# Kernel optimization log

Hardware: AMD Instinct MI355X
Metric: run time of the kernel (lower is better)

The kernel has to match this reference:

```python
import jax, jax.numpy as jnp
import numpy as np

N_NODES = 25000
N_HEDGES = 12500
NNZ = 400000
C_IN = 128
HID = 256
HEADS = 4
DH = HID // HEADS  # 64
NQ = 1             # number_queries
LN_EPS = 1e-5


def _layer_norm(x, g, b):
    m = jnp.mean(x, axis=-1, keepdims=True)
    v = jnp.mean((x - m) ** 2, axis=-1, keepdims=True)
    return (x - m) * jax.lax.rsqrt(v + LN_EPS) * g + b


def _block(x_src, src, tgt, n_tgt, K, Qw, V, ln0_g, ln0_b, ln1_g, ln1_b, W1, W2):
    """AllSetTransformerBlock: segment-softmax multi-head attention + LN/MLP.

    x_src: [N_src, C]; K,V: [H, C, DH]; Qw: [H, NQ, DH]; src,tgt: [E] int.
    torch.sparse.softmax over dim=1 == softmax over each target's incident
    sources (unspecified entries are -inf), so a segment softmax is exact.
    """
    xK = jnp.einsum('nc,hcd->hnd', x_src, K)        # [H, N, DH]
    alpha = jnp.einsum('hqd,hnd->nhq', Qw, xK)      # [N, H, NQ]
    a = alpha[src]                                   # [E, H, NQ] gather per incidence
    m = jax.ops.segment_max(a, tgt, num_segments=n_tgt)
    e = jnp.exp(a - m[tgt])
    den = jax.ops.segment_sum(e, tgt, num_segments=n_tgt)
    attn = e / den[tgt]                              # [E, H, NQ]
    v = jnp.einsum('nc,hcd->nhd', x_src, V)[src]     # [E, H, DH]
    w = attn[:, :, :, None] * v[:, :, None, :]       # [E, H, NQ, DH]
    out = jax.ops.segment_sum(w, tgt, num_segments=n_tgt)  # [T, H, NQ, DH]
    out = out + Qw[None]                             # residual with queries
    out = out.transpose(0, 2, 1, 3).reshape(n_tgt, NQ, HID)
    x = _layer_norm(out, ln0_g, ln0_b)
    h = jnp.maximum(x @ W1, 0.0) @ W2                # MLP: Linear-ReLU-Linear, no bias
    x = _layer_norm(x + jnp.maximum(h, 0.0), ln1_g, ln1_b)
    return x.sum(axis=1)                             # [T, HID]


def setup_inputs() -> dict:
    key = jax.random.key(0)
    ks = jax.random.split(key, 12)
    # injective linear-congruential index generation -> unique (node, hedge) pairs,
    # matching a coalesced sparse incidence matrix
    P = 15485863
    lin = (np.arange(NNZ, dtype=np.int64) * P) % (N_NODES * N_HEDGES)
    node_idx = jnp.asarray(lin // N_HEDGES, dtype=jnp.int64)
    hedge_idx = jnp.asarray(lin % N_HEDGES, dtype=jnp.int64)
    s = 0.05
    w = lambda k, shape: jax.random.normal(k, shape, jnp.float32) * s
    d = {
        'x0': jax.random.normal(ks[0], (N_NODES, C_IN), jnp.float32),
        'node_idx': node_idx,
        'hedge_idx': hedge_idx,
        'n_hedges': N_HEDGES,
        'v2e_K': w(ks[1], (HEADS, C_IN, DH)),
        'v2e_Q': w(ks[2], (HEADS, NQ, DH)),
        'v2e_V': w(ks[3], (HEADS, C_IN, DH)),
        'v2e_W1': w(ks[4], (HID, HID)),
        'v2e_W2': w(ks[5], (HID, HID)),
        'v2e_ln0_g': jnp.ones(HID, jnp.float32), 'v2e_ln0_b': jnp.zeros(HID, jnp.float32),
        'v2e_ln1_g': jnp.ones(HID, jnp.float32), 'v2e_ln1_b': jnp.zeros(HID, jnp.float32),
        'e2v_K': w(ks[6], (HEADS, HID, DH)),
        'e2v_Q': w(ks[7], (HEADS, NQ, DH)),
        'e2v_V': w(ks[8], (HEADS, HID, DH)),
        'e2v_W1': w(ks[9], (HID, HID)),
        'e2v_W2': w(ks[10], (HID, HID)),
        'e2v_ln0_g': jnp.ones(HID, jnp.float32), 'e2v_ln0_b': jnp.zeros(HID, jnp.float32),
        'e2v_ln1_g': jnp.ones(HID, jnp.float32), 'e2v_ln1_b': jnp.zeros(HID, jnp.float32),
    }
    return d


def reference(x0, node_idx, hedge_idx, n_hedges,
              v2e_K, v2e_Q, v2e_V, v2e_W1, v2e_W2,
              v2e_ln0_g, v2e_ln0_b, v2e_ln1_g, v2e_ln1_b,
              e2v_K, e2v_Q, e2v_V, e2v_W1, e2v_W2,
              e2v_ln0_g, e2v_ln0_b, e2v_ln1_g, e2v_ln1_b):
    n_nodes = x0.shape[0]
    # vertex -> hyperedge (neighborhood = B^T: targets are hyperedges)
    x1 = jax.nn.relu(_block(x0, node_idx, hedge_idx, n_hedges,
                            v2e_K, v2e_Q, v2e_V,
                            v2e_ln0_g, v2e_ln0_b, v2e_ln1_g, v2e_ln1_b,
                            v2e_W1, v2e_W2))
    # hyperedge -> vertex (neighborhood = B: targets are nodes)
    x0_out = jax.nn.relu(_block(x1, hedge_idx, node_idx, n_nodes,
                                e2v_K, e2v_Q, e2v_V,
                                e2v_ln0_g, e2v_ln0_b, e2v_ln1_g, e2v_ln1_b,
                                e2v_W1, e2v_W2))
    return x0_out, x1
```

## Files before the change

kernel.cpp:

```cpp
#include <hip/hip_runtime.h>
#include <hip/hip_bf16.h>

#define N_NODES_C 25000
#define N_HEDGES_C 12500
#define NNZ_C 400000
#define C_IN_C 128
#define HID_C 256
#define LN_EPS_C 1e-5f
#define CSR_STRIDE 64

typedef unsigned short ushort_t;
typedef __attribute__((ext_vector_type(8))) short short8;
typedef __attribute__((ext_vector_type(4))) float f32x4;

union U4S8 { uint4 u; short8 s; };

__device__ __forceinline__ float ldsel(const void* p, size_t i, bool f32) {
    return f32 ? ((const float*)p)[i] : __bfloat162float(((const __hip_bfloat16*)p)[i]);
}
__device__ __forceinline__ int ldidx(const void* p, size_t i, bool i64) {
    return i64 ? (int)((const long long*)p)[i] : ((const int*)p)[i];
}
__device__ __forceinline__ ushort_t bfbits(float f) {
    union { float f; unsigned u; } v; v.f = f;
    unsigned r = v.u + 0x7FFF + ((v.u >> 16) & 1);
    return (ushort_t)(r >> 16);
}
__device__ __forceinline__ float blo(unsigned u) {
    union { unsigned u; float f; } v; v.u = u << 16; return v.f;
}
__device__ __forceinline__ float bhi(unsigned u) {
    union { unsigned u; float f; } v; v.u = u & 0xFFFF0000u; return v.f;
}

#define INIT_GRID 148
__global__ void __launch_bounds__(256)
init_kernel(const unsigned* __restrict__ x0w, const unsigned* __restrict__ idxw,
            int* __restrict__ flags, unsigned* __restrict__ cnts,
            unsigned* __restrict__ vb32, unsigned* __restrict__ ea32) {
    int bid = blockIdx.x;
    if (bid == 0) {
        __shared__ int cnt[2];
        int t = threadIdx.x;
        if (t < 2) cnt[t] = 0;
        __syncthreads();
        int c0 = 0, c1 = 0;
        for (int k = 0; k < 4; k++) {
            unsigned w = x0w[t * 4 + k];
            unsigned elo = (w >> 7) & 0xFF;
            if (elo >= 100 && elo <= 134) c0++;
            if (idxw[2 * (t * 4 + k) + 1] == 0) c1++;
        }
        atomicAdd(&cnt[0], c0);
        atomicAdd(&cnt[1], c1);
        __syncthreads();
        if (t == 0) {
            flags[0] = (cnt[0] < 512) ? 1 : 0;
            flags[1] = (cnt[1] >= 512) ? 1 : 0;
        }
        return;
    }
    int i = (bid - 1) * 256 + threadIdx.x;
    if (i < 37500) { cnts[i] = 0u; return; }
    i -= 37500;
    if (i < 128) { vb32[25000 * 128 + i] = 0u; return; }
    i -= 128;
    if (i < 4) ea32[100000 + i] = 0u;
}

#define FILL_CHUNK 1024
#define FILL_NCHUNK ((NNZ_C + FILL_CHUNK - 1) / FILL_CHUNK)
#define FILL_BLOCKS (8 * FILL_NCHUNK)
#define HSLICE_SZ 1563
#define NSLICE_SZ 3125
#define PREP_TOTAL 364544
#define PREP_BLOCKS ((PREP_TOTAL + 255) / 256)
#define PF_GRID (FILL_BLOCKS + PREP_BLOCKS)

__global__ void __launch_bounds__(256)
prep_fill_kernel(const void* __restrict__ node_idx, const void* __restrict__ hedge_idx,
                 int* __restrict__ fill_h, int* __restrict__ fill_n,
                 ushort_t* __restrict__ scsr_h, ushort_t* __restrict__ scsr_n,
                 const void* __restrict__ K1, const void* __restrict__ Q1,
                 const void* __restrict__ V1,
                 const void* __restrict__ K2, const void* __restrict__ Q2,
                 const void* __restrict__ V2,
                 const void* __restrict__ W1a, const void* __restrict__ W2a,
                 const void* __restrict__ W1b, const void* __restrict__ W2b,
                 const void* __restrict__ G0a, const void* __restrict__ B0a,
                 const void* __restrict__ G1a, const void* __restrict__ B1a,
                 const void* __restrict__ G0b, const void* __restrict__ B0b,
                 const void* __restrict__ G1b, const void* __restrict__ B1b,
                 const int* __restrict__ flags,
                 float* __restrict__ kq1, float* __restrict__ kq2,
                 ushort_t* __restrict__ Vt1b, ushort_t* __restrict__ Vt2b,
                 ushort_t* __restrict__ W1tA, ushort_t* __restrict__ W2tA,
                 ushort_t* __restrict__ W1tB, ushort_t* __restrict__ W2tB,
                 float* __restrict__ qgb1, float* __restrict__ ep1,
                 float* __restrict__ qgb2, float* __restrict__ ep2) {
    if (blockIdx.x < FILL_BLOCKS) {
        bool i64 = flags[1] != 0;
        int s = blockIdx.x & 7;
        int chunk = blockIdx.x >> 3;
        int e0 = chunk * FILL_CHUNK;
        int e1 = e0 + FILL_CHUNK; if (e1 > NNZ_C) e1 = NNZ_C;
        int hlo = s * HSLICE_SZ, hhi = hlo + HSLICE_SZ;
        int nlo = s * NSLICE_SZ, nhi = nlo + NSLICE_SZ;
        for (int e = e0 + threadIdx.x; e < e1; e += 256) {
            int nd = ldidx(node_idx, e, i64);
            int he = ldidx(hedge_idx, e, i64);
            if (he >= hlo && he < hhi) {
                int p = atomicAdd(&fill_h[he], 1);
                if (p < CSR_STRIDE) scsr_h[(he << 6) + p] = (ushort_t)nd;
            }
            if (nd >= nlo && nd < nhi) {
                int p = atomicAdd(&fill_n[nd], 1);
                if (p < CSR_STRIDE) scsr_n[(nd << 6) + p] = (ushort_t)he;
            }
        }
        return;
    }
    bool f32 = flags[0] != 0;
    size_t i = (size_t)(blockIdx.x - FILL_BLOCKS) * 256 + threadIdx.x;
    if (i >= PREP_TOTAL) return;
    if (i < 512) {
        int h = (int)(i >> 7), c = (int)(i & 127);
        float s = 0.f;
        for (int d = 0; d < 64; d++)
            s += ldsel(K1, (size_t)(h * 128 + c) * 64 + d, f32) * ldsel(Q1, h * 64 + d, f32);
        kq1[h * 128 + c] = s;
        return;
    }
    i -= 512;
    if (i < 1024) {
        int h = (int)(i >> 8), c = (int)(i & 255);
        float s = 0.f;
        for (int d = 0; d < 64; d++)
            s += ldsel(K2, (size_t)(h * 256 + c) * 64 + d, f32) * ldsel(Q2, h * 64 + d, f32);
        kq2[h * 256 + c] = s;
        return;
    }
    i -= 1024;
    if (i < 32768) {
        int j = (int)(i >> 7), c = (int)(i & 127);
        int h = j >> 6, d = j & 63;
        Vt1b[i] = bfbits(ldsel(V1, (size_t)(h * 128 + c) * 64 + d, f32));
        return;
    }
    i -= 32768;
    if (i < 65536) {
        int j = (int)(i >> 8), c = (int)(i & 255);
        int h = j >> 6, d = j & 63;
        Vt2b[i] = bfbits(ldsel(V2, (size_t)(h * 256 + c) * 64 + d, f32));
        return;
    }
    i -= 65536;
    if (i < 65536) { int n = (int)(i >> 8), k = (int)(i & 255);
        W1tA[i] = bfbits(ldsel(W1a, (size_t)k * 256 + n, f32)); return; }
    i -= 65536;
    if (i < 65536) { int n = (int)(i >> 8), k = (int)(i & 255);
        W2tA[i] = bfbits(ldsel(W2a, (size_t)k * 256 + n, f32)); return; }
    i -= 65536;
    if (i < 65536) { int n = (int)(i >> 8), k = (int)(i & 255);
        W1tB[i] = bfbits(ldsel(W1b, (size_t)k * 256 + n, f32)); return; }
    i -= 65536;
    if (i < 65536) { int n = (int)(i >> 8), k = (int)(i & 255);
        W2tB[i] = bfbits(ldsel(W2b, (size_t)k * 256 + n, f32)); return; }
    i -= 65536;
    {
        int which = (int)(i >> 8);
        int j = (int)(i & 255);
        const void* src; float* dst;
        switch (which) {
            case 0: src = Q1;  dst = qgb1;       break;
            case 1: src = G0a; dst = qgb1 + 256; break;
            case 2: src = B0a; dst = qgb1 + 512; break;
            case 3: src = G1a; dst = ep1;        break;
            case 4: src = B1a; dst = ep1 + 256;  break;
            case 5: src = Q2;  dst = qgb2;       break;
            case 6: src = G0b; dst = qgb2 + 256; break;
            case 7: src = B0b; dst = qgb2 + 512; break;
            case 8: src = G1b; dst = ep2;        break;
            default: src = B1b; dst = ep2 + 256;  break;
        }
        dst[j] = ldsel(src, j, f32);
    }
}

__global__ void __launch_bounds__(256)
gemm_x0_kernel(const void* __restrict__ x0, const int* __restrict__ flags,
               const ushort_t* __restrict__ Bt, ushort_t* __restrict__ C,
               int M, int K, const float* __restrict__ kq, float* __restrict__ ea) {
    __shared__ ushort_t As[64 * 72];
    __shared__ ushort_t Bs[128 * 72];
    __shared__ float kqs[512];
    bool f32 = flags[0] != 0;
    int tid = threadIdx.x;
    int w = tid >> 6, lane = tid & 63;
    int l15 = lane & 15, kg = lane >> 4;
    int wr = w >> 1, wc = w & 1;
    int row0 = blockIdx.x * 64, col0 = blockIdx.y * 128;
    bool doEa = (blockIdx.y == 0);
    kqs[tid] = kq[tid];
    kqs[256 + tid] = kq[256 + tid];
    __syncthreads();
    f32x4 acc[2][4] = {{{0.f,0.f,0.f,0.f},{0.f,0.f,0.f,0.f},{0.f,0.f,0.f,0.f},{0.f,0.f,0.f,0.f}},
                       {{0.f,0.f,0.f,0.f},{0.f,0.f,0.f,0.f},{0.f,0.f,0.f,0.f},{0.f,0.f,0.f,0.f}}};
    float hd[2][4] = {{0.f,0.f,0.f,0.f},{0.f,0.f,0.f,0.f}};
    int r_ = tid >> 3, ch = tid & 7;
    for (int k0 = 0; k0 < K; k0 += 64) {
#pragma unroll
        for (int p = 0; p < 2; p++) {
            int r = p * 32 + r_;
            uint4 av = {0u,0u,0u,0u};
            int gr = row0 + r;
            if (gr < M) {
                float fv[8];
                if (!f32) {
                    av = *(const uint4*)((const ushort_t*)x0 + (size_t)gr * K + k0 + ch * 8);
                    if (doEa) {
                        unsigned* uw = (unsigned*)&av;
#pragma unroll
                        for (int jj = 0; jj < 4; jj++) { fv[2 * jj] = blo(uw[jj]); fv[2 * jj + 1] = bhi(uw[jj]); }
                    }
                } else {
                    const float* ap = (const float*)x0 + (size_t)gr * K + k0 + ch * 8;
                    float4 f0 = *(const float4*)ap;
                    float4 f1 = *(const float4*)(ap + 4);
                    av.x = (unsigned)bfbits(f0.x) | ((unsigned)bfbits(f0.y) << 16);
                    av.y = (unsigned)bfbits(f0.z) | ((unsigned)bfbits(f0.w) << 16);
                    av.z = (unsigned)bfbits(f1.x) | ((unsigned)bfbits(f1.y) << 16);
                    av.w = (unsigned)bfbits(f1.z) | ((unsigned)bfbits(f1.w) << 16);
                    if (doEa) {
                        fv[0] = f0.x; fv[1] = f0.y; fv[2] = f0.z; fv[3] = f0.w;
                        fv[4] = f1.x; fv[5] = f1.y; fv[6] = f1.z; fv[7] = f1.w;
                    }
                }
                if (doEa) {
                    int c = k0 + ch * 8;
#pragma unroll
                    for (int h = 0; h < 4; h++) {
                        float s = 0.f;
#pragma unroll
                        for (int j = 0; j < 8; j++) s += fv[j] * kqs[h * 128 + c + j];
                        hd[p][h] += s;
                    }
                }
            }
            *(uint4*)&As[r * 72 + ch * 8] = av;
        }
#pragma unroll
        for (int p = 0; p < 4; p++) {
            int i = p * 256 + tid;
            int r2 = i >> 3, c2 = i & 7;
            uint4 bv = *(const uint4*)(Bt + (size_t)(col0 + r2) * K + k0 + c2 * 8);
            *(uint4*)&Bs[r2 * 72 + c2 * 8] = bv;
        }
        __syncthreads();
#pragma unroll
        for (int kk = 0; kk < 2; kk++) {
            U4S8 a0_, a1_;
            a0_.u = *(const uint4*)&As[(32 * wr + l15) * 72 + kk * 32 + kg * 8];
            a1_.u = *(const uint4*)&As[(32 * wr + 16 + l15) * 72 + kk * 32 + kg * 8];
#pragma unroll
            for (int n = 0; n < 4; n++) {
                U4S8 b; b.u = *(const uint4*)&Bs[(64 * wc + 16 * n + l15) * 72 + kk * 32 + kg * 8];
                acc[0][n] = __builtin_amdgcn_mfma_f32_16x16x32_bf16(a0_.s, b.s, acc[0][n], 0, 0, 0);
                acc[1][n] = __builtin_amdgcn_mfma_f32_16x16x32_bf16(a1_.s, b.s, acc[1][n], 0, 0, 0);
            }
        }
        __syncthreads();
    }
#pragma unroll
    for (int m = 0; m < 2; m++) {
#pragma unroll
        for (int n = 0; n < 4; n++) {
#pragma unroll
            for (int rr = 0; rr < 4; rr++) {
                int row = row0 + 32 * wr + 16 * m + kg * 4 + rr;
                if (row < M)
                    C[(size_t)row * 256 + col0 + 64 * wc + 16 * n + l15] = bfbits(acc[m][n][rr]);
            }
        }
    }
    if (doEa) {
#pragma unroll
        for (int p = 0; p < 2; p++) {
#pragma unroll
            for (int msk = 1; msk < 8; msk <<= 1) {
                hd[p][0] += __shfl_xor(hd[p][0], msk);
                hd[p][1] += __shfl_xor(hd[p][1], msk);
                hd[p][2] += __shfl_xor(hd[p][2], msk);
                hd[p][3] += __shfl_xor(hd[p][3], msk);
            }
            if (ch == 0) {
                int row = row0 + p * 32 + r_;
                if (row < M) {
                    float4 o;
                    o.x = __expf(hd[p][0]); o.y = __expf(hd[p][1]);
                    o.z = __expf(hd[p][2]); o.w = __expf(hd[p][3]);
                    *(float4*)(ea + (size_t)row * 4) = o;
                }
            }
        }
    }
}

#define LOADB4(SRC, KO) { \
    bv0 = *(const uint4*)((SRC) + (size_t)rb * 256 + (KO) + cb * 8); \
    bv1 = *(const uint4*)((SRC) + (size_t)(rb + 64) * 256 + (KO) + cb * 8); \
    bv2 = *(const uint4*)((SRC) + (size_t)(rb + 128) * 256 + (KO) + cb * 8); \
    bv3 = *(const uint4*)((SRC) + (size_t)(rb + 192) * 256 + (KO) + cb * 8); }
#define WRITEB4() { \
    *(uint4*)&Bs[rb * 72 + cb * 8] = bv0; \
    *(uint4*)&Bs[(rb + 64) * 72 + cb * 8] = bv1; \
    *(uint4*)&Bs[(rb + 128) * 72 + cb * 8] = bv2; \
    *(uint4*)&Bs[(rb + 192) * 72 + cb * 8] = bv3; }

__global__ void __launch_bounds__(512)
fused_mlp_ln_kernel(const ushort_t* __restrict__ A, const ushort_t* __restrict__ W1t,
                    const ushort_t* __restrict__ W2t, const float* __restrict__ ep,
                    float* __restrict__ outF, int M,
                    const ushort_t* __restrict__ Vt2b, const float* __restrict__ kq,
                    ushort_t* __restrict__ vbOut, float* __restrict__ eaOut,
                    unsigned* __restrict__ zrow, float* __restrict__ zea) {
    __shared__ ushort_t Bs[256 * 72];
    __shared__ ushort_t hs[32 * 264];
    __shared__ float s1s[32][4];
    __shared__ float s2s[32][4];
    __shared__ float kqs[1024];
    ushort_t* As = hs;
    int tid = threadIdx.x;
    int w = tid >> 6, lane = tid & 63;
    int l15 = lane & 15, kg = lane >> 4;
    int wr = w >> 2, wc = w & 3;
    int row0 = blockIdx.x * 32;
    bool dir1 = (Vt2b != nullptr);
    if (dir1) { kqs[tid] = kq[tid]; kqs[512 + tid] = kq[512 + tid]; }
    f32x4 acc[4] = {{0.f,0.f,0.f,0.f},{0.f,0.f,0.f,0.f},{0.f,0.f,0.f,0.f},{0.f,0.f,0.f,0.f}};
    int rb = tid >> 3, cb = tid & 7;
    bool doA = tid < 256;
    int gr = row0 + rb;
    uint4 av = {0u,0u,0u,0u};
    uint4 bv0, bv1, bv2, bv3;
    LOADB4(W1t, 0);
    if (doA && gr < M) av = *(const uint4*)(A + (size_t)gr * 256 + cb * 8);
    for (int k0 = 0; k0 < 256; k0 += 64) {
        WRITEB4();
        if (doA) *(uint4*)&As[rb * 72 + cb * 8] = av;
        __syncthreads();
        if (k0 < 192) {
            LOADB4(W1t, k0 + 64);
            if (doA && gr < M) av = *(const uint4*)(A + (size_t)gr * 256 + (k0 + 64) + cb * 8);
        }
#pragma unroll
        for (int kk = 0; kk < 2; kk++) {
            U4S8 a0_;
            a0_.u = *(const uint4*)&As[(16 * wr + l15) * 72 + kk * 32 + kg * 8];
#pragma unroll
            for (int n = 0; n < 4; n++) {
                U4S8 b; b.u = *(const uint4*)&Bs[(64 * wc + 16 * n + l15) * 72 + kk * 32 + kg * 8];
                acc[n] = __builtin_amdgcn_mfma_f32_16x16x32_bf16(a0_.s, b.s, acc[n], 0, 0, 0);
            }
        }
        __syncthreads();
    }
    LOADB4(W2t, 0);
#pragma unroll
    for (int n = 0; n < 4; n++) {
#pragma unroll
        for (int rr = 0; rr < 4; rr++) {
            int br = 16 * wr + kg * 4 + rr;
            hs[br * 264 + 64 * wc + 16 * n + l15] = bfbits(fmaxf(acc[n][rr], 0.f));
            acc[n][rr] = 0.f;
        }
    }
    __syncthreads();
    for (int k0 = 0; k0 < 256; k0 += 64) {
        WRITEB4();
        __syncthreads();
        if (k0 < 192) LOADB4(W2t, k0 + 64);
#pragma unroll
        for (int kk = 0; kk < 2; kk++) {
            U4S8 a0_;
            a0_.u = *(const uint4*)&hs[(16 * wr + l15) * 264 + k0 + kk * 32 + kg * 8];
#pragma unroll
            for (int n = 0; n < 4; n++) {
                U4S8 b; b.u = *(const uint4*)&Bs[(64 * wc + 16 * n + l15) * 72 + kk * 32 + kg * 8];
                acc[n] = __builtin_amdgcn_mfma_f32_16x16x32_bf16(a0_.s, b.s, acc[n], 0, 0, 0);
            }
        }
        __syncthreads();
    }
    float ym[4][4];
#pragma unroll
    for (int rr = 0; rr < 4; rr++) {
        int br = 16 * wr + kg * 4 + rr;
        int grow = row0 + br;
        float ls1 = 0.f;
#pragma unroll
        for (int n = 0; n < 4; n++) {
            int col = 64 * wc + 16 * n + l15;
            float xv = 0.f;
            if (grow < M) xv = blo((unsigned)A[(size_t)grow * 256 + col]);
            float yv = xv + fmaxf(acc[n][rr], 0.f);
            ym[n][rr] = yv;
            ls1 += yv;
        }
#pragma unroll
        for (int msk = 1; msk < 16; msk <<= 1) ls1 += __shfl_xor(ls1, msk);
        if (l15 == 0) s1s[br][wc] = ls1;
    }
    __syncthreads();
    float mean_[4];
#pragma unroll
    for (int rr = 0; rr < 4; rr++) {
        int br = 16 * wr + kg * 4 + rr;
        float mn = (s1s[br][0] + s1s[br][1] + s1s[br][2] + s1s[br][3]) * (1.f / 256.f);
        mean_[rr] = mn;
        float ls2 = 0.f;
#pragma unroll
        for (int n = 0; n < 4; n++) {
            float d = ym[n][rr] - mn;
            ls2 += d * d;
        }
#pragma unroll
        for (int msk = 1; msk < 16; msk <<= 1) ls2 += __shfl_xor(ls2, msk);
        if (l15 == 0) s2s[br][wc] = ls2;
    }
    __syncthreads();
#pragma unroll
    for (int rr = 0; rr < 4; rr++) {
        int br = 16 * wr + kg * 4 + rr;
        int grow = row0 + br;
        float var = (s2s[br][0] + s2s[br][1] + s2s[br][2] + s2s[br][3]) * (1.f / 256.f);
        float rs = rsqrtf(var + LN_EPS_C);
#pragma unroll
        for (int n = 0; n < 4; n++) {
            int col = 64 * wc + 16 * n + l15;
            float rv = (ym[n][rr] - mean_[rr]) * rs * ep[col] + ep[256 + col];
            rv = fmaxf(rv, 0.f);
            if (grow < M) outF[(size_t)grow * 256 + col] = rv;
            if (dir1) hs[br * 264 + col] = bfbits(rv);
        }
    }
    if (!dir1) return;
#pragma unroll
    for (int n = 0; n < 4; n++)
#pragma unroll
        for (int rr = 0; rr < 4; rr++) acc[n][rr] = 0.f;
    LOADB4(Vt2b, 0);
    __syncthreads();
    if (blockIdx.x == 0) {
        if (tid < 128) zrow[tid] = 0u;
        else if (tid < 132) zea[tid - 128] = 0.f;
    }
    {
        int rrow = tid >> 4, rch = tid & 15;
        float h0 = 0.f, h1 = 0.f, h2 = 0.f, h3 = 0.f;
#pragma unroll
        for (int q = 0; q < 2; q++) {
            uint4 xv = *(const uint4*)&hs[rrow * 264 + rch * 16 + q * 8];
            const unsigned* uw = (const unsigned*)&xv;
#pragma unroll
            for (int jj = 0; jj < 4; jj++) {
                float xl = blo(uw[jj]), xh = bhi(uw[jj]);
                int c = rch * 16 + q * 8 + jj * 2;
                h0 += xl * kqs[c]       + xh * kqs[c + 1];
                h1 += xl * kqs[256 + c] + xh * kqs[256 + c + 1];
                h2 += xl * kqs[512 + c] + xh * kqs[512 + c + 1];
                h3 += xl * kqs[768 + c] + xh * kqs[768 + c + 1];
            }
        }
#pragma unroll
        for (int msk = 1; msk < 16; msk <<= 1) {
            h0 += __shfl_xor(h0, msk); h1 += __shfl_xor(h1, msk);
            h2 += __shfl_xor(h2, msk); h3 += __shfl_xor(h3, msk);
        }
        int grow = row0 + rrow;
        if (rch == 0 && grow < M) {
            float4 o;
            o.x = __expf(h0); o.y = __expf(h1); o.z = __expf(h2); o.w = __expf(h3);
            *(float4*)(eaOut + (size_t)grow * 4) = o;
        }
    }
    for (int k0 = 0; k0 < 256; k0 += 64) {
        WRITEB4();
        __syncthreads();
        if (k0 < 192) LOADB4(Vt2b, k0 + 64);
#pragma unroll
        for (int kk = 0; kk < 2; kk++) {
            U4S8 a0_;
            a0_.u = *(const uint4*)&hs[(16 * wr + l15) * 264 + k0 + kk * 32 + kg * 8];
#pragma unroll
            for (int n = 0; n < 4; n++) {
                U4S8 b; b.u = *(const uint4*)&Bs[(64 * wc + 16 * n + l15) * 72 + kk * 32 + kg * 8];
                acc[n] = __builtin_amdgcn_mfma_f32_16x16x32_bf16(a0_.s, b.s, acc[n], 0, 0, 0);
            }
        }
        __syncthreads();
    }
#pragma unroll
    for (int n = 0; n < 4; n++) {
#pragma unroll
        for (int rr = 0; rr < 4; rr++) {
            int row = row0 + 16 * wr + kg * 4 + rr;
            if (row < M)
                vbOut[(size_t)row * 256 + 64 * wc + 16 * n + l15] = bfbits(acc[n][rr]);
        }
    }
}

#define DECL_BANKD(B) float e##B##0, e##B##1, e##B##2, e##B##3; \
                      uint2 u##B##0, u##B##1, u##B##2, u##B##3;
#define ISSUED1(B, n, sl) { \
    int _i = ((sl) < cnt) ? __shfl(myidx, (sl)) : dummyIdx; \
    int _o = _i << 9; \
    u##B##n = *(const uint2*)(vbL + _o); \
    e##B##n = *(const float*)(eaL + (_o >> 5)); }
#define ISSUED4(B, base) ISSUED1(B,0,(base)) ISSUED1(B,1,(base)+1) ISSUED1(B,2,(base)+2) ISSUED1(B,3,(base)+3)
#define EATD1(B, n) { \
    float wgt = e##B##n; \
    den += wgt; \
    a0 += wgt * blo(u##B##n.x); a1 += wgt * bhi(u##B##n.x); \
    a2 += wgt * blo(u##B##n.y); a3 += wgt * bhi(u##B##n.y); }
#define EATD4(B) EATD1(B,0) EATD1(B,1) EATD1(B,2) EATD1(B,3)

__global__ void __launch_bounds__(256)
attn_ln_kernel(const int* __restrict__ cnts, const ushort_t* __restrict__ scsr,
               const char* __restrict__ eaB, const char* __restrict__ vbB,
               const float* __restrict__ qgb, uint2* __restrict__ xlnbf2,
               int dummyIdx) {
    int wid = (blockIdx.x << 2) + (threadIdx.x >> 6);
    int lane = threadIdx.x & 63;
    const char* vbL = vbB + (lane << 3);
    const char* eaL = eaB + ((lane >> 4) << 2);
    int cnt = cnts[wid];
    if (cnt > CSR_STRIDE) cnt = CSR_STRIDE;
    int myidx = (int)scsr[(wid << 6) + lane];
    float a0 = 0.f, a1 = 0.f, a2 = 0.f, a3 = 0.f, den = 0.f;
    int kr = (cnt + 3) & ~3;
    DECL_BANKD(A)
    DECL_BANKD(B)
    if (kr > 0) { ISSUED4(A, 0) }
    for (int k = 0; k < kr; k += 8) {
        int kb = k + 4;
        bool hasB = kb < kr;
        if (hasB) { ISSUED4(B, kb) }
        EATD4(A)
        int ka = k + 8;
        if (ka < kr) { ISSUED4(A, ka) }
        if (hasB) { EATD4(B) }
    }
    float inv = (den > 0.f) ? (1.f / den) : 0.f;
    int c0i = lane << 2;
    float o0 = a0 * inv + qgb[c0i];
    float o1 = a1 * inv + qgb[c0i + 1];
    float o2 = a2 * inv + qgb[c0i + 2];
    float o3 = a3 * inv + qgb[c0i + 3];
    float part = o0 + o1 + o2 + o3;
#pragma unroll
    for (int m = 32; m; m >>= 1) part += __shfl_xor(part, m);
    float mean = part * (1.f / 256.f);
    float d0 = o0 - mean, d1 = o1 - mean, d2 = o2 - mean, d3 = o3 - mean;
    float p2 = d0 * d0 + d1 * d1 + d2 * d2 + d3 * d3;
#pragma unroll
    for (int m = 32; m; m >>= 1) p2 += __shfl_xor(p2, m);
    float rs = rsqrtf(p2 * (1.f / 256.f) + LN_EPS_C);
    float r0 = d0 * rs * qgb[256 + c0i] + qgb[512 + c0i];
    float r1 = d1 * rs * qgb[256 + c0i + 1] + qgb[512 + c0i + 1];
    float r2 = d2 * rs * qgb[256 + c0i + 2] + qgb[512 + c0i + 2];
    float r3 = d3 * rs * qgb[256 + c0i + 3] + qgb[512 + c0i + 3];
    uint2 outw;
    outw.x = ((unsigned)bfbits(r1) << 16) | bfbits(r0);
    outw.y = ((unsigned)bfbits(r3) << 16) | bfbits(r2);
    xlnbf2[(size_t)wid * 64 + lane] = outw;
}

#define OFF_KQ1   0
#define OFF_KQ2   2048
#define OFF_QGB1  6144
#define OFF_EP1   9216
#define OFF_QGB2  11264
#define OFF_EP2   14336
#define OFF_EA    16384
#define OFF_VT1B  416512
#define OFF_VT2B  482048
#define OFF_W1TA  613120
#define OFF_W2TA  744192
#define OFF_W1TB  875264
#define OFF_W2TB  1006336
#define OFF_VB    1137408
#define OFF_XLNBF 13937920
#define OFF_FLAGS 45937920
#define OFF_FILLH 45937952
#define OFF_FILLN 45987952
#define OFF_SCSRH 46087952
#define OFF_SCSRN 47687952

extern "C" void kernel_launch(void* const* d_in, const int* in_sizes, int n_in,
                              void* d_out, int out_size, void* d_ws, size_t ws_size,
                              hipStream_t stream) {
    const void* x0        = d_in[0];
    const void* node_idx  = d_in[1];
    const void* hedge_idx = d_in[2];
    const void* v2e_K  = d_in[4];
    const void* v2e_Q  = d_in[5];
    const void* v2e_V  = d_in[6];
    const void* v2e_W1 = d_in[7];
    const void* v2e_W2 = d_in[8];
    const void* v2e_ln0_g = d_in[9];
    const void* v2e_ln0_b = d_in[10];
    const void* v2e_ln1_g = d_in[11];
    const void* v2e_ln1_b = d_in[12];
    const void* e2v_K  = d_in[13];
    const void* e2v_Q  = d_in[14];
    const void* e2v_V  = d_in[15];
    const void* e2v_W1 = d_in[16];
    const void* e2v_W2 = d_in[17];
    const void* e2v_ln0_g = d_in[18];
    const void* e2v_ln0_b = d_in[19];
    const void* e2v_ln1_g = d_in[20];
    const void* e2v_ln1_b = d_in[21];

    float* out = (float*)d_out;
    float* out_x0 = out;
    float* out_x1 = out + (size_t)N_NODES_C * HID_C;

    char* base = (char*)d_ws;
    float*    kq1   = (float*)(base + OFF_KQ1);
    float*    kq2   = (float*)(base + OFF_KQ2);
    float*    qgb1  = (float*)(base + OFF_QGB1);
    float*    ep1   = (float*)(base + OFF_EP1);
    float*    qgb2  = (float*)(base + OFF_QGB2);
    float*    ep2   = (float*)(base + OFF_EP2);
    float*    ea    = (float*)(base + OFF_EA);
    ushort_t* Vt1b  = (ushort_t*)(base + OFF_VT1B);
    ushort_t* Vt2b  = (ushort_t*)(base + OFF_VT2B);
    ushort_t* W1tA  = (ushort_t*)(base + OFF_W1TA);
    ushort_t* W2tA  = (ushort_t*)(base + OFF_W2TA);
    ushort_t* W1tB  = (ushort_t*)(base + OFF_W1TB);
    ushort_t* W2tB  = (ushort_t*)(base + OFF_W2TB);
    ushort_t* vb    = (ushort_t*)(base + OFF_VB);
    ushort_t* xlnbf = (ushort_t*)(base + OFF_XLNBF);
    int*      flags = (int*)(base + OFF_FLAGS);
    int*      fill_h = (int*)(base + OFF_FILLH);
    int*      fill_n = (int*)(base + OFF_FILLN);
    ushort_t* scsr_h = (ushort_t*)(base + OFF_SCSRH);
    ushort_t* scsr_n = (ushort_t*)(base + OFF_SCSRN);

    init_kernel<<<INIT_GRID, 256, 0, stream>>>(
        (const unsigned*)x0, (const unsigned*)node_idx, flags,
        (unsigned*)fill_h, (unsigned*)vb, (unsigned*)ea);

    prep_fill_kernel<<<PF_GRID, 256, 0, stream>>>(
        node_idx, hedge_idx, fill_h, fill_n, scsr_h, scsr_n,
        v2e_K, v2e_Q, v2e_V, e2v_K, e2v_Q, e2v_V,
        v2e_W1, v2e_W2, e2v_W1, e2v_W2,
        v2e_ln0_g, v2e_ln0_b, v2e_ln1_g, v2e_ln1_b,
        e2v_ln0_g, e2v_ln0_b, e2v_ln1_g, e2v_ln1_b,
        flags, kq1, kq2, Vt1b, Vt2b, W1tA, W2tA, W1tB, W2tB,
        qgb1, ep1, qgb2, ep2);

    gemm_x0_kernel<<<dim3((N_NODES_C + 63) / 64, 2), 256, 0, stream>>>(
        x0, flags, Vt1b, vb, N_NODES_C, C_IN_C, kq1, ea);
    attn_ln_kernel<<<N_HEDGES_C / 4, 256, 0, stream>>>(
        fill_h, scsr_h, (const char*)ea, (const char*)vb, qgb1, (uint2*)xlnbf,
        25000);
    fused_mlp_ln_kernel<<<(N_HEDGES_C + 31) / 32, 512, 0, stream>>>(
        xlnbf, W1tA, W2tA, ep1, out_x1, N_HEDGES_C,
        Vt2b, kq2, vb, ea,
        (unsigned*)vb + 12500 * 128, ea + 50000);

    attn_ln_kernel<<<N_NODES_C / 4, 256, 0, stream>>>(
        fill_n, scsr_n, (const char*)ea, (const char*)vb, qgb2, (uint2*)xlnbf,
        12500);
    fused_mlp_ln_kernel<<<(N_NODES_C + 31) / 32, 512, 0, stream>>>(
        xlnbf, W1tB, W2tB, ep2, out_x0, N_NODES_C,
        nullptr, nullptr, nullptr, nullptr, nullptr, nullptr);
}
```

Before: 182.8 us.

## Fuse first-layer x0 GEMM into prep/fill megakernel, reading V1 directly

```diff
diff --git a/kernel.cpp b/kernel.cpp
--- a/kernel.cpp
+++ b/kernel.cpp
@@ -73,31 +73,37 @@
 #define FILL_BLOCKS (8 * FILL_NCHUNK)
 #define HSLICE_SZ 1563
 #define NSLICE_SZ 3125
-#define PREP_TOTAL 364544
-#define PREP_BLOCKS ((PREP_TOTAL + 255) / 256)
-#define PF_GRID (FILL_BLOCKS + PREP_BLOCKS)
+#define GEMM_BLOCKS (2 * ((N_NODES_C + 63) / 64))
+#define PREP_TOTAL 331264
+#define PREP_BLOCKS (PREP_TOTAL / 256)
+#define MEGA_GRID (FILL_BLOCKS + GEMM_BLOCKS + PREP_BLOCKS)
 
 __global__ void __launch_bounds__(256)
-prep_fill_kernel(const void* __restrict__ node_idx, const void* __restrict__ hedge_idx,
-                 int* __restrict__ fill_h, int* __restrict__ fill_n,
-                 ushort_t* __restrict__ scsr_h, ushort_t* __restrict__ scsr_n,
-                 const void* __restrict__ K1, const void* __restrict__ Q1,
-                 const void* __restrict__ V1,
-                 const void* __restrict__ K2, const void* __restrict__ Q2,
-                 const void* __restrict__ V2,
-                 const void* __restrict__ W1a, const void* __restrict__ W2a,
-                 const void* __restrict__ W1b, const void* __restrict__ W2b,
-                 const void* __restrict__ G0a, const void* __restrict__ B0a,
-                 const void* __restrict__ G1a, const void* __restrict__ B1a,
-                 const void* __restrict__ G0b, const void* __restrict__ B0b,
-                 const void* __restrict__ G1b, const void* __restrict__ B1b,
-                 const int* __restrict__ flags,
-                 float* __restrict__ kq1, float* __restrict__ kq2,
-                 ushort_t* __restrict__ Vt1b, ushort_t* __restrict__ Vt2b,
-                 ushort_t* __restrict__ W1tA, ushort_t* __restrict__ W2tA,
-                 ushort_t* __restrict__ W1tB, ushort_t* __restrict__ W2tB,
-                 float* __restrict__ qgb1, float* __restrict__ ep1,
-                 float* __restrict__ qgb2, float* __restrict__ ep2) {
+mega_kernel(const void* __restrict__ node_idx, const void* __restrict__ hedge_idx,
+            int* __restrict__ fill_h, int* __restrict__ fill_n,
+            ushort_t* __restrict__ scsr_h, ushort_t* __restrict__ scsr_n,
+            const void* __restrict__ x0, ushort_t* __restrict__ vbC,
+            float* __restrict__ ea,
+            const void* __restrict__ K1, const void* __restrict__ Q1,
+            const void* __restrict__ V1,
+            const void* __restrict__ K2, const void* __restrict__ Q2,
+            const void* __restrict__ V2,
+            const void* __restrict__ W1a, const void* __restrict__ W2a,
+            const void* __restrict__ W1b, const void* __restrict__ W2b,
+            const void* __restrict__ G0a, const void* __restrict__ B0a,
+            const void* __restrict__ G1a, const void* __restrict__ B1a,
+            const void* __restrict__ G0b, const void* __restrict__ B0b,
+            const void* __restrict__ G1b, const void* __restrict__ B1b,
+            const int* __restrict__ flags,
+            float* __restrict__ kq2,
+            ushort_t* __restrict__ Vt2b,
+            ushort_t* __restrict__ W1tA, ushort_t* __restrict__ W2tA,
+            ushort_t* __restrict__ W1tB, ushort_t* __restrict__ W2tB,
+            float* __restrict__ qgb1, float* __restrict__ ep1,
+            float* __restrict__ qgb2, float* __restrict__ ep2) {
+    __shared__ ushort_t As[64 * 72];
+    __shared__ ushort_t Bs[128 * 72];
+    __shared__ float kqs[512];
     if (blockIdx.x < FILL_BLOCKS) {
         bool i64 = flags[1] != 0;
         int s = blockIdx.x & 7;
@@ -120,18 +126,156 @@
         }
         return;
     }
+    if (blockIdx.x < FILL_BLOCKS + GEMM_BLOCKS) {
+        int gi = blockIdx.x - FILL_BLOCKS;
+        int bx = gi >> 1, by = gi & 1;
+        int row0 = bx * 64, col0 = by * 128;
+        bool doEa = (by == 0);
+        bool f32 = flags[0] != 0;
+        int tid = threadIdx.x;
+        int w = tid >> 6, lane = tid & 63;
+        int l15 = lane & 15, kg = lane >> 4;
+        int wr = w >> 1, wc = w & 1;
+        int h0 = col0 >> 6;
+        if (doEa) {
+            for (int i = tid; i < 512; i += 256) {
+                int h = i >> 7, c = i & 127;
+                float s = 0.f;
+                for (int d = 0; d < 64; d++)
+                    s += ldsel(K1, (size_t)(h * 128 + c) * 64 + d, f32) * ldsel(Q1, h * 64 + d, f32);
+                kqs[i] = s;
+            }
+        }
+        __syncthreads();
+        f32x4 acc[2][4] = {{{0.f,0.f,0.f,0.f},{0.f,0.f,0.f,0.f},{0.f,0.f,0.f,0.f},{0.f,0.f,0.f,0.f}},
+                           {{0.f,0.f,0.f,0.f},{0.f,0.f,0.f,0.f},{0.f,0.f,0.f,0.f},{0.f,0.f,0.f,0.f}}};
+        float hd[2][4] = {{0.f,0.f,0.f,0.f},{0.f,0.f,0.f,0.f}};
+        int r_ = tid >> 3, ch = tid & 7;
+        for (int k0 = 0; k0 < C_IN_C; k0 += 64) {
+#pragma unroll
+            for (int p = 0; p < 2; p++) {
+                int r = p * 32 + r_;
+                uint4 av = {0u,0u,0u,0u};
+                int gr = row0 + r;
+                if (gr < N_NODES_C) {
+                    float fv[8];
+                    if (!f32) {
+                        av = *(const uint4*)((const ushort_t*)x0 + (size_t)gr * C_IN_C + k0 + ch * 8);
+                        if (doEa) {
+                            unsigned* uw = (unsigned*)&av;
+#pragma unroll
+                            for (int jj = 0; jj < 4; jj++) { fv[2 * jj] = blo(uw[jj]); fv[2 * jj + 1] = bhi(uw[jj]); }
+                        }
+                    } else {
+                        const float* ap = (const float*)x0 + (size_t)gr * C_IN_C + k0 + ch * 8;
+                        float4 f0 = *(const float4*)ap;
+                        float4 f1 = *(const float4*)(ap + 4);
+                        av.x = (unsigned)bfbits(f0.x) | ((unsigned)bfbits(f0.y) << 16);
+                        av.y = (unsigned)bfbits(f0.z) | ((unsigned)bfbits(f0.w) << 16);
+                        av.z = (unsigned)bfbits(f1.x) | ((unsigned)bfbits(f1.y) << 16);
+                        av.w = (unsigned)bfbits(f1.z) | ((unsigned)bfbits(f1.w) << 16);
+                        if (doEa) {
+                            fv[0] = f0.x; fv[1] = f0.y; fv[2] = f0.z; fv[3] = f0.w;
+                            fv[4] = f1.x; fv[5] = f1.y; fv[6] = f1.z; fv[7] = f1.w;
+                        }
+                    }
+                    if (doEa) {
+                        int c = k0 + ch * 8;
+#pragma unroll
+                        for (int h = 0; h < 4; h++) {
+                            float s = 0.f;
+#pragma unroll
+                            for (int j = 0; j < 8; j++) s += fv[j] * kqs[h * 128 + c + j];
+                            hd[p][h] += s;
+                        }
+                    }
+                }
+                *(uint4*)&As[r * 72 + ch * 8] = av;
+            }
+            if (!f32) {
+#pragma unroll
+                for (int q = 0; q < 2; q++) {
+                    const ushort_t* vsrc = (const ushort_t*)V1 + ((size_t)(h0 + q) * 128 + k0) * 64;
+#pragma unroll
+                    for (int p = 0; p < 2; p++) {
+                        int eidx = (p * 256 + tid) * 8;
+                        int cr = eidx >> 6, d = eidx & 63;
+                        uint4 v = *(const uint4*)(vsrc + eidx);
+                        const ushort_t* vs = (const ushort_t*)&v;
+#pragma unroll
+                        for (int jj = 0; jj < 8; jj++)
+                            Bs[(q * 64 + d + jj) * 72 + cr] = vs[jj];
+                    }
+                }
+            } else {
+#pragma unroll
+                for (int q = 0; q < 2; q++) {
+                    const float* vsrc = (const float*)V1 + ((size_t)(h0 + q) * 128 + k0) * 64;
+#pragma unroll
+                    for (int p = 0; p < 4; p++) {
+                        int eidx = (p * 256 + tid) * 4;
+                        int cr = eidx >> 6, d = eidx & 63;
+                        float4 f = *(const float4*)(vsrc + eidx);
+                        Bs[(q * 64 + d + 0) * 72 + cr] = bfbits(f.x);
+                        Bs[(q * 64 + d + 1) * 72 + cr] = bfbits(f.y);
+                        Bs[(q * 64 + d + 2) * 72 + cr] = bfbits(f.z);
+                        Bs[(q * 64 + d + 3) * 72 + cr] = bfbits(f.w);
+                    }
+                }
+            }
+            __syncthreads();
+#pragma unroll
+            for (int kk = 0; kk < 2; kk++) {
+                U4S8 a0_, a1_;
+                a0_.u = *(const uint4*)&As[(32 * wr + l15) * 72 + kk * 32 + kg * 8];
+                a1_.u = *(const uint4*)&As[(32 * wr + 16 + l15) * 72 + kk * 32 + kg * 8];
+#pragma unroll
+                for (int n = 0; n < 4; n++) {
+                    U4S8 b; b.u = *(const uint4*)&Bs[(64 * wc + 16 * n + l15) * 72 + kk * 32 + kg * 8];
+                    acc[0][n] = __builtin_amdgcn_mfma_f32_16x16x32_bf16(a0_.s, b.s, acc[0][n], 0, 0, 0);
+                    acc[1][n] = __builtin_amdgcn_mfma_f32_16x16x32_bf16(a1_.s, b.s, acc[1][n], 0, 0, 0);
+                }
+            }
+            __syncthreads();
+        }
+#pragma unroll
+        for (int m = 0; m < 2; m++) {
+#pragma unroll
+            for (int n = 0; n < 4; n++) {
+#pragma unroll
+                for (int rr = 0; rr < 4; rr++) {
+                    int row = row0 + 32 * wr + 16 * m + kg * 4 + rr;
+                    if (row < N_NODES_C)
+                        vbC[(size_t)row * 256 + col0 + 64 * wc + 16 * n + l15] = bfbits(acc[m][n][rr]);
+                }
+            }
+        }
+        if (doEa) {
+#pragma unroll
+            for (int p = 0; p < 2; p++) {
+#pragma unroll
+                for (int msk = 1; msk < 8; msk <<= 1) {
+                    hd[p][0] += __shfl_xor(hd[p][0], msk);
+                    hd[p][1] += __shfl_xor(hd[p][1], msk);
+                    hd[p][2] += __shfl_xor(hd[p][2], msk);
+                    hd[p][3] += __shfl_xor(hd[p][3], msk);
+                }
+                if (ch == 0) {
+                    int row = row0 + p * 32 + r_;
+                    if (row < N_NODES_C) {
+                        float4 o;
+                        o.x = __expf(hd[p][0]); o.y = __expf(hd[p][1]);
+                        o.z = __expf(hd[p][2]); o.w = __expf(hd[p][3]);
+                        *(float4*)(ea + (size_t)row * 4) = o;
+                    }
+                }
+            }
+        }
+        return;
+    }
     bool f32 = flags[0] != 0;
-    size_t i = (size_t)(blockIdx.x - FILL_BLOCKS) * 256 + threadIdx.x;
+    size_t i = (size_t)(blockIdx.x - FILL_BLOCKS - GEMM_BLOCKS) * 256 + threadIdx.x;
     if (i >= PREP_TOTAL) return;
-    if (i < 512) {
-        int h = (int)(i >> 7), c = (int)(i & 127);
-        float s = 0.f;
-        for (int d = 0; d < 64; d++)
-            s += ldsel(K1, (size_t)(h * 128 + c) * 64 + d, f32) * ldsel(Q1, h * 64 + d, f32);
-        kq1[h * 128 + c] = s;
-        return;
-    }
-    i -= 512;
     if (i < 1024) {
         int h = (int)(i >> 8), c = (int)(i & 255);
         float s = 0.f;
@@ -141,13 +285,6 @@
         return;
     }
     i -= 1024;
-    if (i < 32768) {
-        int j = (int)(i >> 7), c = (int)(i & 127);
-        int h = j >> 6, d = j & 63;
-        Vt1b[i] = bfbits(ldsel(V1, (size_t)(h * 128 + c) * 64 + d, f32));
-        return;
-    }
-    i -= 32768;
     if (i < 65536) {
         int j = (int)(i >> 8), c = (int)(i & 255);
         int h = j >> 6, d = j & 63;
@@ -184,125 +321,6 @@
             default: src = B1b; dst = ep2 + 256;  break;
         }
         dst[j] = ldsel(src, j, f32);
-    }
-}
-
-__global__ void __launch_bounds__(256)
-gemm_x0_kernel(const void* __restrict__ x0, const int* __restrict__ flags,
-               const ushort_t* __restrict__ Bt, ushort_t* __restrict__ C,
-               int M, int K, const float* __restrict__ kq, float* __restrict__ ea) {
-    __shared__ ushort_t As[64 * 72];
-    __shared__ ushort_t Bs[128 * 72];
-    __shared__ float kqs[512];
-    bool f32 = flags[0] != 0;
-    int tid = threadIdx.x;
-    int w = tid >> 6, lane = tid & 63;
-    int l15 = lane & 15, kg = lane >> 4;
-    int wr = w >> 1, wc = w & 1;
-    int row0 = blockIdx.x * 64, col0 = blockIdx.y * 128;
-    bool doEa = (blockIdx.y == 0);
-    kqs[tid] = kq[tid];
-    kqs[256 + tid] = kq[256 + tid];
-    __syncthreads();
-    f32x4 acc[2][4] = {{{0.f,0.f,0.f,0.f},{0.f,0.f,0.f,0.f},{0.f,0.f,0.f,0.f},{0.f,0.f,0.f,0.f}},
-                       {{0.f,0.f,0.f,0.f},{0.f,0.f,0.f,0.f},{0.f,0.f,0.f,0.f},{0.f,0.f,0.f,0.f}}};
-    float hd[2][4] = {{0.f,0.f,0.f,0.f},{0.f,0.f,0.f,0.f}};
-    int r_ = tid >> 3, ch = tid & 7;
-    for (int k0 = 0; k0 < K; k0 += 64) {
-#pragma unroll
-        for (int p = 0; p < 2; p++) {
-            int r = p * 32 + r_;
-            uint4 av = {0u,0u,0u,0u};
-            int gr = row0 + r;
-            if (gr < M) {
-                float fv[8];
-                if (!f32) {
-                    av = *(const uint4*)((const ushort_t*)x0 + (size_t)gr * K + k0 + ch * 8);
-                    if (doEa) {
-                        unsigned* uw = (unsigned*)&av;
-#pragma unroll
-                        for (int jj = 0; jj < 4; jj++) { fv[2 * jj] = blo(uw[jj]); fv[2 * jj + 1] = bhi(uw[jj]); }
-                    }
-                } else {
-                    const float* ap = (const float*)x0 + (size_t)gr * K + k0 + ch * 8;
-                    float4 f0 = *(const float4*)ap;
-                    float4 f1 = *(const float4*)(ap + 4);
-                    av.x = (unsigned)bfbits(f0.x) | ((unsigned)bfbits(f0.y) << 16);
-                    av.y = (unsigned)bfbits(f0.z) | ((unsigned)bfbits(f0.w) << 16);
-                    av.z = (unsigned)bfbits(f1.x) | ((unsigned)bfbits(f1.y) << 16);
-                    av.w = (unsigned)bfbits(f1.z) | ((unsigned)bfbits(f1.w) << 16);
-                    if (doEa) {
-                        fv[0] = f0.x; fv[1] = f0.y; fv[2] = f0.z; fv[3] = f0.w;
-                        fv[4] = f1.x; fv[5] = f1.y; fv[6] = f1.z; fv[7] = f1.w;
-                    }
-                }
-                if (doEa) {
-                    int c = k0 + ch * 8;
-#pragma unroll
-                    for (int h = 0; h < 4; h++) {
-                        float s = 0.f;
-#pragma unroll
-                        for (int j = 0; j < 8; j++) s += fv[j] * kqs[h * 128 + c + j];
-                        hd[p][h] += s;
-                    }
-                }
-            }
-            *(uint4*)&As[r * 72 + ch * 8] = av;
-        }
-#pragma unroll
-        for (int p = 0; p < 4; p++) {
-            int i = p * 256 + tid;
-            int r2 = i >> 3, c2 = i & 7;
-            uint4 bv = *(const uint4*)(Bt + (size_t)(col0 + r2) * K + k0 + c2 * 8);
-            *(uint4*)&Bs[r2 * 72 + c2 * 8] = bv;
-        }
-        __syncthreads();
-#pragma unroll
-        for (int kk = 0; kk < 2; kk++) {
-            U4S8 a0_, a1_;
-            a0_.u = *(const uint4*)&As[(32 * wr + l15) * 72 + kk * 32 + kg * 8];
-            a1_.u = *(const uint4*)&As[(32 * wr + 16 + l15) * 72 + kk * 32 + kg * 8];
-#pragma unroll
-            for (int n = 0; n < 4; n++) {
-                U4S8 b; b.u = *(const uint4*)&Bs[(64 * wc + 16 * n + l15) * 72 + kk * 32 + kg * 8];
-                acc[0][n] = __builtin_amdgcn_mfma_f32_16x16x32_bf16(a0_.s, b.s, acc[0][n], 0, 0, 0);
-                acc[1][n] = __builtin_amdgcn_mfma_f32_16x16x32_bf16(a1_.s, b.s, acc[1][n], 0, 0, 0);
-            }
-        }
-        __syncthreads();
-    }
-#pragma unroll
-    for (int m = 0; m < 2; m++) {
-#pragma unroll
-        for (int n = 0; n < 4; n++) {
-#pragma unroll
-            for (int rr = 0; rr < 4; rr++) {
-                int row = row0 + 32 * wr + 16 * m + kg * 4 + rr;
-                if (row < M)
-                    C[(size_t)row * 256 + col0 + 64 * wc + 16 * n + l15] = bfbits(acc[m][n][rr]);
-            }
-        }
-    }
-    if (doEa) {
-#pragma unroll
-        for (int p = 0; p < 2; p++) {
-#pragma unroll
-            for (int msk = 1; msk < 8; msk <<= 1) {
-                hd[p][0] += __shfl_xor(hd[p][0], msk);
-                hd[p][1] += __shfl_xor(hd[p][1], msk);
-                hd[p][2] += __shfl_xor(hd[p][2], msk);
-                hd[p][3] += __shfl_xor(hd[p][3], msk);
-            }
-            if (ch == 0) {
-                int row = row0 + p * 32 + r_;
-                if (row < M) {
-                    float4 o;
-                    o.x = __expf(hd[p][0]); o.y = __expf(hd[p][1]);
-                    o.z = __expf(hd[p][2]); o.w = __expf(hd[p][3]);
-                    *(float4*)(ea + (size_t)row * 4) = o;
-                }
-            }
-        }
     }
 }
 
@@ -577,14 +595,12 @@
     xlnbf2[(size_t)wid * 64 + lane] = outw;
 }
 
-#define OFF_KQ1   0
 #define OFF_KQ2   2048
 #define OFF_QGB1  6144
 #define OFF_EP1   9216
 #define OFF_QGB2  11264
 #define OFF_EP2   14336
 #define OFF_EA    16384
-#define OFF_VT1B  416512
 #define OFF_VT2B  482048
 #define OFF_W1TA  613120
 #define OFF_W2TA  744192
@@ -628,14 +644,12 @@
     float* out_x1 = out + (size_t)N_NODES_C * HID_C;
 
     char* base = (char*)d_ws;
-    float*    kq1   = (float*)(base + OFF_KQ1);
     float*    kq2   = (float*)(base + OFF_KQ2);
     float*    qgb1  = (float*)(base + OFF_QGB1);
     float*    ep1   = (float*)(base + OFF_EP1);
     float*    qgb2  = (float*)(base + OFF_QGB2);
     float*    ep2   = (float*)(base + OFF_EP2);
     float*    ea    = (float*)(base + OFF_EA);
-    ushort_t* Vt1b  = (ushort_t*)(base + OFF_VT1B);
     ushort_t* Vt2b  = (ushort_t*)(base + OFF_VT2B);
     ushort_t* W1tA  = (ushort_t*)(base + OFF_W1TA);
     ushort_t* W2tA  = (ushort_t*)(base + OFF_W2TA);
@@ -653,17 +667,16 @@
         (const unsigned*)x0, (const unsigned*)node_idx, flags,
         (unsigned*)fill_h, (unsigned*)vb, (unsigned*)ea);
 
-    prep_fill_kernel<<<PF_GRID, 256, 0, stream>>>(
+    mega_kernel<<<MEGA_GRID, 256, 0, stream>>>(
         node_idx, hedge_idx, fill_h, fill_n, scsr_h, scsr_n,
+        x0, vb, ea,
         v2e_K, v2e_Q, v2e_V, e2v_K, e2v_Q, e2v_V,
         v2e_W1, v2e_W2, e2v_W1, e2v_W2,
         v2e_ln0_g, v2e_ln0_b, v2e_ln1_g, v2e_ln1_b,
         e2v_ln0_g, e2v_ln0_b, e2v_ln1_g, e2v_ln1_b,
-        flags, kq1, kq2, Vt1b, Vt2b, W1tA, W2tA, W1tB, W2tB,
+        flags, kq2, Vt2b, W1tA, W2tA, W1tB, W2tB,
         qgb1, ep1, qgb2, ep2);
 
-    gemm_x0_kernel<<<dim3((N_NODES_C + 63) / 64, 2), 256, 0, stream>>>(
-        x0, flags, Vt1b, vb, N_NODES_C, C_IN_C, kq1, ea);
     attn_ln_kernel<<<N_HEDGES_C / 4, 256, 0, stream>>>(
         fill_h, scsr_h, (const char*)ea, (const char*)vb, qgb1, (uint2*)xlnbf,
         25000);
```

Result: slower. 241.8 us (+32.3%).
